# Kernel optimization log

Measured on AMD Instinct MI355X. Metric: run time of the kernel, lower is better.

The kernel has to match this reference:

```python
import jax, jax.numpy as jnp
import numpy as np

# NOTE: the original torch code writes `torch.tensor(10 ^ -18)` which is Python
# bitwise XOR, i.e. the constant -28 (NOT 1e-18). We replicate that exact math.
RULE_OFFSET = -28.0


def setup_inputs() -> dict:
    key = jax.random.key(0)
    k0, k1, k2, k3 = jax.random.split(key, 4)
    batch, n_rules, n_fea = 8192, 256, 128
    data = jax.random.normal(k0, (batch, n_fea), dtype=jnp.float32)
    para_mu = jax.random.uniform(k1, (n_rules, n_fea), dtype=jnp.float32)
    para_sigma = jax.random.uniform(k2, (n_rules, n_fea), dtype=jnp.float32)
    para_w3 = jax.random.uniform(k3, (n_rules, n_fea + 1), dtype=jnp.float32)
    return {"data": data, "para_mu": para_mu, "para_sigma": para_sigma, "para_w3": para_w3}


def reference(data, para_mu, para_sigma, para_w3):
    # Gaussian fuzzification exponents: (batch, n_rules, n_fea)
    diff = data[:, None, :] - para_mu[None, :, :]
    exponent = -(diff ** 2) / (2.0 * para_sigma ** 2)
    # prod over features of exp(.) == exp(sum over features) -- same math, fused.
    layer_rule = jnp.exp(jnp.sum(exponent, axis=2))  # (batch, n_rules)
    layer_rule = layer_rule + RULE_OFFSET
    inv_frn = 1.0 / jnp.sum(layer_rule, axis=1, keepdims=True)  # (batch, 1)
    layer_normalize = layer_rule * inv_frn  # (batch, n_rules)
    # TSK consequent: w3[:,0] + sum_f w3[:,1:] * x
    layer_conq = para_w3[:, 0][None, :] + jnp.einsum('bf,rf->br', data, para_w3[:, 1:])
    layer_out_tsk = jnp.sum(layer_normalize * layer_conq, axis=1)  # (batch,)
    return jax.nn.sigmoid(layer_out_tsk)
```

## Files before the change

### kernel.cpp

```cpp
#include <hip/hip_runtime.h>
#include <math.h>

#define NR 256
#define NF 128
#define BCOLS 32

typedef short  s16x8  __attribute__((ext_vector_type(8)));
typedef __bf16 bf16x8 __attribute__((ext_vector_type(8)));
typedef float  f32x16 __attribute__((ext_vector_type(16)));

__device__ __forceinline__ unsigned short f2bf(float x) {
    unsigned int u = __float_as_uint(x);
    unsigned int r = (u + 0x7FFFu + ((u >> 16) & 1u)) >> 16;
    return (unsigned short)r;
}
__device__ __forceinline__ float bf2f(unsigned short b) {
    return __uint_as_float(((unsigned int)b) << 16);
}
__device__ __forceinline__ bf16x8 as_bf(s16x8 v) {
    return __builtin_bit_cast(bf16x8, v);
}
__device__ __forceinline__ f32x16 mfma_bf16(s16x8 a, s16x8 b, f32x16 acc) {
    return __builtin_amdgcn_mfma_f32_32x32x16_bf16(as_bf(a), as_bf(b), acc, 0, 0, 0);
}

__global__ __launch_bounds__(128) void prep_kernel(
    const float* __restrict__ mu, const float* __restrict__ sigma,
    const float* __restrict__ w3,
    unsigned short* __restrict__ PH, unsigned short* __restrict__ PL,
    unsigned short* __restrict__ WC,
    float* __restrict__ Cr, float* __restrict__ W0)
{
    const int r = blockIdx.x;
    const int f = threadIdx.x;
    const size_t i = (size_t)r * NF + f;
    const float s  = sigma[i];
    const float m  = mu[i];
    const float u2 = -0.5f / fmaxf(s * s, 1e-30f);
    const float u1 = -2.0f * u2 * m;
    const float w  = w3[(size_t)r * (NF + 1) + 1 + f];

    const unsigned short ah = f2bf(u2); const unsigned short al = f2bf(u2 - bf2f(ah));
    const unsigned short bh = f2bf(u1); const unsigned short bl = f2bf(u1 - bf2f(bh));
    const unsigned short wh = f2bf(w);  const unsigned short wl = f2bf(w  - bf2f(wh));

    const int rt   = r >> 5;
    const int rc   = r & 31;
    const int ks   = f >> 4;
    const int k16  = f & 15;
    const int lane = (k16 >> 3) * 32 + rc;
    const int j    = k16 & 7;
    const size_t idx1 = ((size_t)((rt * 16 + ks)     * 64) + lane) * 8 + j;
    const size_t idx2 = ((size_t)((rt * 16 + 8 + ks) * 64) + lane) * 8 + j;
    PH[idx1] = ah;  PH[idx2] = bh;
    PL[idx1] = al;  PL[idx2] = bl;
    WC[idx1] = wh;  WC[idx2] = wl;

    float cc = u2 * m * m;
    #pragma unroll
    for (int off = 32; off > 0; off >>= 1) cc += __shfl_down(cc, off);
    __shared__ float tmp[2];
    if ((f & 63) == 0) tmp[f >> 6] = cc;
    __syncthreads();
    if (f == 0) {
        Cr[r] = tmp[0] + tmp[1];
        W0[r] = w3[(size_t)r * (NF + 1)];
    }
}

__global__ __launch_bounds__(512) void fnn_mfma(
    const float* __restrict__ data,
    const unsigned short* __restrict__ PH, const unsigned short* __restrict__ PL,
    const unsigned short* __restrict__ WC,
    const float* __restrict__ Cr, const float* __restrict__ W0,
    float* __restrict__ out)
{
    __shared__ s16x8 sBH[16][64], sBL[16][64];
    __shared__ float sCr[NR], sW0[NR];
    __shared__ float redD[8][BCOLS], redN[8][BCOLS];

    const int tid = threadIdx.x;
    if (tid < NR) sCr[tid] = Cr[tid];
    else          sW0[tid - NR] = W0[tid - NR];

    const int b0 = blockIdx.x * BCOLS;

    {
        const int bks = tid >> 6;
        const int bln = tid & 63;
        const float* p = data + (size_t)(b0 + (bln & 31)) * NF
                              + bks * 16 + (bln >> 5) * 8;
        const float4 v0 = *(const float4*)(p);
        const float4 v1 = *(const float4*)(p + 4);
        const float dv[8] = {v0.x, v0.y, v0.z, v0.w, v1.x, v1.y, v1.z, v1.w};
        s16x8 e_d, e_dl, e_d2, e_d2l;
        #pragma unroll
        for (int j = 0; j < 8; ++j) {
            const float d  = dv[j];
            const float d2 = d * d;
            const unsigned short dh  = f2bf(d);
            const unsigned short d2h = f2bf(d2);
            e_d  [j] = (short)dh;
            e_dl [j] = (short)f2bf(d  - bf2f(dh));
            e_d2 [j] = (short)d2h;
            e_d2l[j] = (short)f2bf(d2 - bf2f(d2h));
        }
        sBH[bks    ][bln] = e_d2;
        sBL[bks    ][bln] = e_d2l;
        sBH[bks + 8][bln] = e_d;
        sBL[bks + 8][bln] = e_dl;
    }
    __syncthreads();

    const int wv   = tid >> 6;
    const int lane = tid & 63;
    const int col  = lane & 31;
    const int half = lane >> 5;

    const s16x8* PHp = (const s16x8*)PH + (size_t)wv * 16 * 64 + lane;
    const s16x8* PLp = (const s16x8*)PL + (size_t)wv * 16 * 64 + lane;
    const s16x8* WCp = (const s16x8*)WC + (size_t)wv * 16 * 64 + lane;

    f32x16 accS0, accS1, accQ;
    #pragma unroll
    for (int e = 0; e < 16; ++e) { accS0[e] = 0.f; accS1[e] = 0.f; accQ[e] = 0.f; }

    s16x8 a0 = PHp[0], a1 = PLp[0], a2 = WCp[0];
    #pragma unroll 1
    for (int ks = 0; ks < 16; ++ks) {
        const int nofs = ((ks < 15) ? (ks + 1) : ks) * 64;
        const s16x8 n0 = PHp[nofs];
        const s16x8 n1 = PLp[nofs];
        const s16x8 n2 = WCp[nofs];

        const s16x8 bh = sBH[ks][lane];
        const s16x8 bl = sBL[ks][lane];
        accS0 = mfma_bf16(a0, bh, accS0);
        accS1 = mfma_bf16(a1, bh, accS1);
        accS1 = mfma_bf16(a0, bl, accS1);
        if (ks < 8) {
            accQ = mfma_bf16(a2, sBH[ks + 8][lane], accQ);
            accQ = mfma_bf16(a2, sBL[ks + 8][lane], accQ);
        } else {
            accQ = mfma_bf16(a2, bh, accQ);
        }
        a0 = n0; a1 = n1; a2 = n2;
    }

    float den_p = 0.f, num_p = 0.f;
    #pragma unroll
    for (int reg = 0; reg < 16; ++reg) {
        const int rloc = (reg & 3) + 8 * (reg >> 2) + 4 * half;
        const int rule = wv * 32 + rloc;
        const float S  = accS0[reg] + accS1[reg] + sCr[rule];
        const float rv = __expf(fminf(S, 0.f)) - 28.0f;
        const float cq = accQ[reg] + sW0[rule];
        den_p += rv;
        num_p += rv * cq;
    }
    den_p += __shfl_xor(den_p, 32);
    num_p += __shfl_xor(num_p, 32);
    if (half == 0) { redD[wv][col] = den_p; redN[wv][col] = num_p; }
    __syncthreads();

    if (tid < BCOLS) {
        float den = 0.f, num = 0.f;
        #pragma unroll
        for (int w = 0; w < 8; ++w) { den += redD[w][tid]; num += redN[w][tid]; }
        out[b0 + tid] = 1.0f / (1.0f + __expf(-(num / den)));
    }
}

#define TBF 8
__global__ __launch_bounds__(256) void fnn_fused(
    const float* __restrict__ data,
    const float* __restrict__ mu, const float* __restrict__ sigma,
    const float* __restrict__ w3,
    float* __restrict__ out)
{
    __shared__ float d_tile[TBF][NF];
    __shared__ float red[TBF][2][4];

    const int tid = threadIdx.x;
    const int b0  = blockIdx.x * TBF;
    {
        const float4* src = (const float4*)(data + (size_t)b0 * NF);
        ((float4*)(&d_tile[0][0]))[tid] = src[tid];
    }
    __syncthreads();

    const float* mu_r = mu    + (size_t)tid * NF;
    const float* sg_r = sigma + (size_t)tid * NF;
    const float* w_r  = w3    + (size_t)tid * (NF + 1);

    float S[TBF], Q[TBF];
    #pragma unroll
    for (int b = 0; b < TBF; ++b) { S[b] = 0.f; Q[b] = 0.f; }

    #pragma unroll 2
    for (int f = 0; f < NF; f += 4) {
        const float4 m4 = *(const float4*)(mu_r + f);
        const float4 s4 = *(const float4*)(sg_r + f);
        const float w0 = w_r[1 + f + 0], w1 = w_r[1 + f + 1];
        const float w2 = w_r[1 + f + 2], w3v = w_r[1 + f + 3];
        float4 c4;
        c4.x = -0.5f / fmaxf(s4.x * s4.x, 1e-30f);
        c4.y = -0.5f / fmaxf(s4.y * s4.y, 1e-30f);
        c4.z = -0.5f / fmaxf(s4.z * s4.z, 1e-30f);
        c4.w = -0.5f / fmaxf(s4.w * s4.w, 1e-30f);
        #pragma unroll
        for (int b = 0; b < TBF; ++b) {
            const float4 d4 = *(const float4*)(&d_tile[b][f]);
            float t;
            t = d4.x - m4.x; S[b] = fmaf(t * t, c4.x, S[b]); Q[b] = fmaf(d4.x, w0,  Q[b]);
            t = d4.y - m4.y; S[b] = fmaf(t * t, c4.y, S[b]); Q[b] = fmaf(d4.y, w1,  Q[b]);
            t = d4.z - m4.z; S[b] = fmaf(t * t, c4.z, S[b]); Q[b] = fmaf(d4.z, w2,  Q[b]);
            t = d4.w - m4.w; S[b] = fmaf(t * t, c4.w, S[b]); Q[b] = fmaf(d4.w, w3v, Q[b]);
        }
    }

    const float bias = w_r[0];
    #pragma unroll
    for (int b = 0; b < TBF; ++b) {
        float rule = __expf(S[b]) - 28.0f;
        float rc   = rule * (bias + Q[b]);
        #pragma unroll
        for (int off = 32; off > 0; off >>= 1) {
            rule += __shfl_down(rule, off);
            rc   += __shfl_down(rc,   off);
        }
        if ((tid & 63) == 0) {
            red[b][0][tid >> 6] = rule;
            red[b][1][tid >> 6] = rc;
        }
    }
    __syncthreads();
    if (tid < TBF) {
        const float den = red[tid][0][0] + red[tid][0][1] + red[tid][0][2] + red[tid][0][3];
        const float num = red[tid][1][0] + red[tid][1][1] + red[tid][1][2] + red[tid][1][3];
        out[b0 + tid] = 1.0f / (1.0f + __expf(-(num / den)));
    }
}

extern "C" void kernel_launch(void* const* d_in, const int* in_sizes, int n_in,
                              void* d_out, int out_size, void* d_ws, size_t ws_size,
                              hipStream_t stream) {
    const float* data  = (const float*)d_in[0];
    const float* mu    = (const float*)d_in[1];
    const float* sigma = (const float*)d_in[2];
    const float* w3    = (const float*)d_in[3];
    float* out = (float*)d_out;

    const int batch = in_sizes[0] / NF;
    const size_t need = 3u * 65536u * sizeof(unsigned short) + 2u * NR * sizeof(float);

    if (ws_size >= need && (batch % BCOLS) == 0) {
        unsigned short* PH = (unsigned short*)d_ws;
        unsigned short* PL = PH + 65536;
        unsigned short* WC = PL + 65536;
        float* Cr = (float*)(WC + 65536);
        float* W0 = Cr + NR;
        prep_kernel<<<NR, NF, 0, stream>>>(mu, sigma, w3, PH, PL, WC, Cr, W0);
        fnn_mfma<<<batch / BCOLS, 512, 0, stream>>>(data, PH, PL, WC, Cr, W0, out);
    } else {
        fnn_fused<<<batch / TBF, 256, 0, stream>>>(data, mu, sigma, w3, out);
    }
}
```

Measured before the change: 18.20 us.

## Vectorize parameter prep kernel and pair k-steps in MFMA main loop

The prep kernel is rebuilt so each thread builds a whole 8-element bf16 fragment and writes it with one 16-byte store, instead of scattered 2-byte stores. The Cr/W0 reductions move into separate blocks that use float4 loads, which shrinks the grid from 256 blocks to 40. The main MFMA loop now handles two k-slices per iteration (ks and ks+8), halving the iteration count and giving more independent MFMAs per iteration to hide latency. The cost is more registers for the doubled prefetch and some redundant reciprocal computation in prep.

```diff
diff --git a/kernel.cpp b/kernel.cpp
--- a/kernel.cpp
+++ b/kernel.cpp
@@ -24,47 +24,69 @@
     return __builtin_amdgcn_mfma_f32_32x32x16_bf16(as_bf(a), as_bf(b), acc, 0, 0, 0);
 }
 
-__global__ __launch_bounds__(128) void prep_kernel(
+__global__ __launch_bounds__(256) void prep2_kernel(
     const float* __restrict__ mu, const float* __restrict__ sigma,
     const float* __restrict__ w3,
     unsigned short* __restrict__ PH, unsigned short* __restrict__ PL,
     unsigned short* __restrict__ WC,
     float* __restrict__ Cr, float* __restrict__ W0)
 {
-    const int r = blockIdx.x;
-    const int f = threadIdx.x;
-    const size_t i = (size_t)r * NF + f;
-    const float s  = sigma[i];
-    const float m  = mu[i];
-    const float u2 = -0.5f / fmaxf(s * s, 1e-30f);
-    const float u1 = -2.0f * u2 * m;
-    const float w  = w3[(size_t)r * (NF + 1) + 1 + f];
-
-    const unsigned short ah = f2bf(u2); const unsigned short al = f2bf(u2 - bf2f(ah));
-    const unsigned short bh = f2bf(u1); const unsigned short bl = f2bf(u1 - bf2f(bh));
-    const unsigned short wh = f2bf(w);  const unsigned short wl = f2bf(w  - bf2f(wh));
-
-    const int rt   = r >> 5;
-    const int rc   = r & 31;
-    const int ks   = f >> 4;
-    const int k16  = f & 15;
-    const int lane = (k16 >> 3) * 32 + rc;
-    const int j    = k16 & 7;
-    const size_t idx1 = ((size_t)((rt * 16 + ks)     * 64) + lane) * 8 + j;
-    const size_t idx2 = ((size_t)((rt * 16 + 8 + ks) * 64) + lane) * 8 + j;
-    PH[idx1] = ah;  PH[idx2] = bh;
-    PL[idx1] = al;  PL[idx2] = bl;
-    WC[idx1] = wh;  WC[idx2] = wl;
-
-    float cc = u2 * m * m;
-    #pragma unroll
-    for (int off = 32; off > 0; off >>= 1) cc += __shfl_down(cc, off);
-    __shared__ float tmp[2];
-    if ((f & 63) == 0) tmp[f >> 6] = cc;
-    __syncthreads();
-    if (f == 0) {
-        Cr[r] = tmp[0] + tmp[1];
-        W0[r] = w3[(size_t)r * (NF + 1)];
+    const int blk = blockIdx.x;
+    if (blk < 32) {
+        const int t    = blk * 256 + threadIdx.x;
+        const int e    = t >> 6;
+        const int lane = t & 63;
+        const int rt   = e >> 4;
+        const int ks2  = e & 15;
+        const bool second = (ks2 >= 8);
+        const int fb   = (ks2 & 7) * 16 + (lane >> 5) * 8;
+        const int rule = rt * 32 + (lane & 31);
+
+        const float* mrow = mu    + (size_t)rule * NF + fb;
+        const float* srow = sigma + (size_t)rule * NF + fb;
+        const float* wrow = w3    + (size_t)rule * (NF + 1) + 1 + fb;
+
+        s16x8 vh, vl, vw;
+        #pragma unroll
+        for (int j = 0; j < 8; ++j) {
+            const float s  = srow[j];
+            const float m  = mrow[j];
+            const float w  = wrow[j];
+            const float u2 = -0.5f / fmaxf(s * s, 1e-30f);
+            const float val = second ? (-2.0f * u2 * m) : u2;
+            const unsigned short hh = f2bf(val);
+            vh[j] = (short)hh;
+            vl[j] = (short)f2bf(val - bf2f(hh));
+            const unsigned short wh = f2bf(w);
+            vw[j] = (short)(second ? f2bf(w - bf2f(wh)) : wh);
+        }
+        ((s16x8*)PH)[t] = vh;
+        ((s16x8*)PL)[t] = vl;
+        ((s16x8*)WC)[t] = vw;
+    } else {
+        const int rg   = blk - 32;
+        const int rl   = threadIdx.x >> 3;
+        const int jj   = threadIdx.x & 7;
+        const int rule = rg * 32 + rl;
+        const float* mrow = mu    + (size_t)rule * NF + jj * 16;
+        const float* srow = sigma + (size_t)rule * NF + jj * 16;
+        float cc = 0.f;
+        #pragma unroll
+        for (int q = 0; q < 16; q += 4) {
+            const float4 s4 = *(const float4*)(srow + q);
+            const float4 m4 = *(const float4*)(mrow + q);
+            cc += (-0.5f / fmaxf(s4.x * s4.x, 1e-30f)) * m4.x * m4.x;
+            cc += (-0.5f / fmaxf(s4.y * s4.y, 1e-30f)) * m4.y * m4.y;
+            cc += (-0.5f / fmaxf(s4.z * s4.z, 1e-30f)) * m4.z * m4.z;
+            cc += (-0.5f / fmaxf(s4.w * s4.w, 1e-30f)) * m4.w * m4.w;
+        }
+        cc += __shfl_down(cc, 4);
+        cc += __shfl_down(cc, 2);
+        cc += __shfl_down(cc, 1);
+        if (jj == 0) {
+            Cr[rule] = cc;
+            W0[rule] = w3[(size_t)rule * (NF + 1)];
+        }
     }
 }
 
@@ -125,26 +147,33 @@
     #pragma unroll
     for (int e = 0; e < 16; ++e) { accS0[e] = 0.f; accS1[e] = 0.f; accQ[e] = 0.f; }
 
-    s16x8 a0 = PHp[0], a1 = PLp[0], a2 = WCp[0];
+    s16x8 aH0 = PHp[0], aH1 = PHp[8 * 64];
+    s16x8 aL0 = PLp[0], aL1 = PLp[8 * 64];
+    s16x8 aW0 = WCp[0], aW1 = WCp[8 * 64];
+
     #pragma unroll 1
-    for (int ks = 0; ks < 16; ++ks) {
-        const int nofs = ((ks < 15) ? (ks + 1) : ks) * 64;
-        const s16x8 n0 = PHp[nofs];
-        const s16x8 n1 = PLp[nofs];
-        const s16x8 n2 = WCp[nofs];
-
-        const s16x8 bh = sBH[ks][lane];
-        const s16x8 bl = sBL[ks][lane];
-        accS0 = mfma_bf16(a0, bh, accS0);
-        accS1 = mfma_bf16(a1, bh, accS1);
-        accS1 = mfma_bf16(a0, bl, accS1);
-        if (ks < 8) {
-            accQ = mfma_bf16(a2, sBH[ks + 8][lane], accQ);
-            accQ = mfma_bf16(a2, sBL[ks + 8][lane], accQ);
-        } else {
-            accQ = mfma_bf16(a2, bh, accQ);
-        }
-        a0 = n0; a1 = n1; a2 = n2;
+    for (int km = 0; km < 8; ++km) {
+        const int kn = (km < 7) ? (km + 1) : km;
+        const s16x8 nH0 = PHp[kn * 64],       nH1 = PHp[(kn + 8) * 64];
+        const s16x8 nL0 = PLp[kn * 64],       nL1 = PLp[(kn + 8) * 64];
+        const s16x8 nW0 = WCp[kn * 64],       nW1 = WCp[(kn + 8) * 64];
+
+        const s16x8 d2h = sBH[km][lane];
+        const s16x8 d2l = sBL[km][lane];
+        const s16x8 dh  = sBH[km + 8][lane];
+        const s16x8 dl  = sBL[km + 8][lane];
+
+        accS0 = mfma_bf16(aH0, d2h, accS0);
+        accS1 = mfma_bf16(aL0, d2h, accS1);
+        accS1 = mfma_bf16(aH0, d2l, accS1);
+        accS0 = mfma_bf16(aH1, dh,  accS0);
+        accS1 = mfma_bf16(aL1, dh,  accS1);
+        accS1 = mfma_bf16(aH1, dl,  accS1);
+        accQ  = mfma_bf16(aW0, dh,  accQ);
+        accQ  = mfma_bf16(aW0, dl,  accQ);
+        accQ  = mfma_bf16(aW1, dh,  accQ);
+
+        aH0 = nH0; aH1 = nH1; aL0 = nL0; aL1 = nL1; aW0 = nW0; aW1 = nW1;
     }
 
     float den_p = 0.f, num_p = 0.f;
@@ -260,7 +289,7 @@
         unsigned short* WC = PL + 65536;
         float* Cr = (float*)(WC + 65536);
         float* W0 = Cr + NR;
-        prep_kernel<<<NR, NF, 0, stream>>>(mu, sigma, w3, PH, PL, WC, Cr, W0);
+        prep2_kernel<<<40, 256, 0, stream>>>(mu, sigma, w3, PH, PL, WC, Cr, W0);
         fnn_mfma<<<batch / BCOLS, 512, 0, stream>>>(data, PH, PL, WC, Cr, W0, out);
     } else {
         fnn_fused<<<batch / TBF, 256, 0, stream>>>(data, mu, sigma, w3, out);
```

New measurement: 22.01 us. 1.21x slower.

## Stage prep parameter packing through LDS and write coalesced 16-byte vectors

Applied to the files above, without the earlier changes.

The parameter-prep kernel now runs 8 blocks of 512 threads, one per 32-rule tile, instead of 256 blocks of 128 threads. Each thread loads 8 contiguous mu/sigma values with float4 loads and writes the bf16 hi/lo MFMA-layout values into shared memory. After a barrier, each tile is copied to global memory as coalesced 16-byte vectors, replacing the scattered 2-byte stores. The row reduction now uses xor shuffles within 16 lanes instead of a shared-memory two-wave reduction. The aim is to cut the prep kernel's uncoalesced-store and launch cost, at the price of only 8 blocks' worth of parallelism.

```diff
diff --git a/kernel.cpp b/kernel.cpp
--- a/kernel.cpp
+++ b/kernel.cpp
@@ -24,47 +24,84 @@
     return __builtin_amdgcn_mfma_f32_32x32x16_bf16(as_bf(a), as_bf(b), acc, 0, 0, 0);
 }
 
-__global__ __launch_bounds__(128) void prep_kernel(
+__global__ __launch_bounds__(512) void prep3_kernel(
     const float* __restrict__ mu, const float* __restrict__ sigma,
     const float* __restrict__ w3,
     unsigned short* __restrict__ PH, unsigned short* __restrict__ PL,
     unsigned short* __restrict__ WC,
     float* __restrict__ Cr, float* __restrict__ W0)
 {
-    const int r = blockIdx.x;
-    const int f = threadIdx.x;
-    const size_t i = (size_t)r * NF + f;
-    const float s  = sigma[i];
-    const float m  = mu[i];
-    const float u2 = -0.5f / fmaxf(s * s, 1e-30f);
-    const float u1 = -2.0f * u2 * m;
-    const float w  = w3[(size_t)r * (NF + 1) + 1 + f];
-
-    const unsigned short ah = f2bf(u2); const unsigned short al = f2bf(u2 - bf2f(ah));
-    const unsigned short bh = f2bf(u1); const unsigned short bl = f2bf(u1 - bf2f(bh));
-    const unsigned short wh = f2bf(w);  const unsigned short wl = f2bf(w  - bf2f(wh));
-
-    const int rt   = r >> 5;
-    const int rc   = r & 31;
-    const int ks   = f >> 4;
-    const int k16  = f & 15;
-    const int lane = (k16 >> 3) * 32 + rc;
-    const int j    = k16 & 7;
-    const size_t idx1 = ((size_t)((rt * 16 + ks)     * 64) + lane) * 8 + j;
-    const size_t idx2 = ((size_t)((rt * 16 + 8 + ks) * 64) + lane) * 8 + j;
-    PH[idx1] = ah;  PH[idx2] = bh;
-    PL[idx1] = al;  PL[idx2] = bl;
-    WC[idx1] = wh;  WC[idx2] = wl;
-
-    float cc = u2 * m * m;
-    #pragma unroll
-    for (int off = 32; off > 0; off >>= 1) cc += __shfl_down(cc, off);
-    __shared__ float tmp[2];
-    if ((f & 63) == 0) tmp[f >> 6] = cc;
-    __syncthreads();
-    if (f == 0) {
-        Cr[r] = tmp[0] + tmp[1];
-        W0[r] = w3[(size_t)r * (NF + 1)];
+    __shared__ unsigned short sH[16 * 64 * 8];
+    __shared__ unsigned short sL[16 * 64 * 8];
+    __shared__ unsigned short sW[16 * 64 * 8];
+
+    const int rt = blockIdx.x;
+    const int t  = threadIdx.x;
+    const int rl = t >> 4;
+    const int rule = rt * 32 + rl;
+    const int f0 = (t & 15) * 8;
+
+    const float* mrow = mu    + (size_t)rule * NF + f0;
+    const float* srow = sigma + (size_t)rule * NF + f0;
+    const float* wrow = w3    + (size_t)rule * (NF + 1) + 1 + f0;
+
+    const float4 m40 = *(const float4*)(mrow);
+    const float4 m41 = *(const float4*)(mrow + 4);
+    const float4 s40 = *(const float4*)(srow);
+    const float4 s41 = *(const float4*)(srow + 4);
+    const float mv[8] = {m40.x, m40.y, m40.z, m40.w, m41.x, m41.y, m41.z, m41.w};
+    const float sv[8] = {s40.x, s40.y, s40.z, s40.w, s41.x, s41.y, s41.z, s41.w};
+
+    const int ks   = f0 >> 4;
+    const int lane = ((f0 >> 3) & 1) * 32 + rl;
+    const int base1 = (ks       * 64 + lane) * 8;
+    const int base2 = ((ks + 8) * 64 + lane) * 8;
+
+    float cc = 0.f;
+    #pragma unroll
+    for (int j = 0; j < 8; ++j) {
+        const float s  = sv[j];
+        const float m  = mv[j];
+        const float w  = wrow[j];
+        const float u2 = -0.5f / fmaxf(s * s, 1e-30f);
+        const float u1 = -2.0f * u2 * m;
+        cc += u2 * m * m;
+
+        const unsigned short u2h = f2bf(u2);
+        const unsigned short u1h = f2bf(u1);
+        const unsigned short wh  = f2bf(w);
+        sH[base1 + j] = u2h;
+        sL[base1 + j] = f2bf(u2 - bf2f(u2h));
+        sW[base1 + j] = wh;
+        sH[base2 + j] = u1h;
+        sL[base2 + j] = f2bf(u1 - bf2f(u1h));
+        sW[base2 + j] = f2bf(w - bf2f(wh));
+    }
+
+    cc += __shfl_xor(cc, 1);
+    cc += __shfl_xor(cc, 2);
+    cc += __shfl_xor(cc, 4);
+    cc += __shfl_xor(cc, 8);
+    if ((t & 15) == 0) {
+        Cr[rule] = cc;
+        W0[rule] = w3[(size_t)rule * (NF + 1)];
+    }
+
+    __syncthreads();
+
+    {
+        s16x8* gH = (s16x8*)PH + (size_t)rt * 1024;
+        s16x8* gL = (s16x8*)PL + (size_t)rt * 1024;
+        s16x8* gW = (s16x8*)WC + (size_t)rt * 1024;
+        const s16x8* lH = (const s16x8*)sH;
+        const s16x8* lL = (const s16x8*)sL;
+        const s16x8* lW = (const s16x8*)sW;
+        gH[t]       = lH[t];
+        gH[t + 512] = lH[t + 512];
+        gL[t]       = lL[t];
+        gL[t + 512] = lL[t + 512];
+        gW[t]       = lW[t];
+        gW[t + 512] = lW[t + 512];
     }
 }
 
@@ -260,7 +297,7 @@
         unsigned short* WC = PL + 65536;
         float* Cr = (float*)(WC + 65536);
         float* W0 = Cr + NR;
-        prep_kernel<<<NR, NF, 0, stream>>>(mu, sigma, w3, PH, PL, WC, Cr, W0);
+        prep3_kernel<<<8, 512, 0, stream>>>(mu, sigma, w3, PH, PL, WC, Cr, W0);
         fnn_mfma<<<batch / BCOLS, 512, 0, stream>>>(data, PH, PL, WC, Cr, W0, out);
     } else {
         fnn_fused<<<batch / TBF, 256, 0, stream>>>(data, mu, sigma, w3, out);
```

After: 18.58 us. 1.02x slower.
